# Kernel tuning notes

Measured on AMD Instinct MI355X. Metric: run time of the kernel, lower is better.

## Reference

```python
import jax, jax.numpy as jnp
import numpy as np

STATE_DIM = 2
HIDDEN = 1024
N_SKILLS = 5
N_ACTIONS = 4
BATCH = 65536


def setup_inputs() -> dict:
    key = jax.random.key(0)
    ks = jax.random.split(key, 8)
    def lin_init(k, fan_in, shape):
        bound = 1.0 / np.sqrt(fan_in)
        return jax.random.uniform(k, shape, jnp.float32, -bound, bound)
    return {
        "s": jax.random.normal(ks[0], (BATCH, STATE_DIM), jnp.float32),
        "skill_idx": jax.random.randint(ks[1], (BATCH,), 0, N_SKILLS, jnp.int32),
        "W1": lin_init(ks[2], STATE_DIM, (STATE_DIM, HIDDEN)),
        "b1": lin_init(ks[3], STATE_DIM, (HIDDEN,)),
        "W2": lin_init(ks[4], HIDDEN, (HIDDEN, HIDDEN)),
        "b2": lin_init(ks[5], HIDDEN, (HIDDEN,)),
        "W_heads": lin_init(ks[6], HIDDEN, (N_SKILLS, HIDDEN, N_ACTIONS)),
        "b_heads": lin_init(ks[7], HIDDEN, (N_SKILLS, N_ACTIONS)),
    }


def reference(s, skill_idx, W1, b1, W2, b2, W_heads, b_heads):
    # shared feature MLP: Linear -> ReLU -> Linear -> ReLU
    h = jax.nn.relu(s @ W1 + b1)            # [B, H]
    feat = jax.nn.relu(h @ W2 + b2)         # [B, H]
    # per-sample skill head: gather weights then one batched contraction
    Wg = W_heads[skill_idx]                 # [B, H, A]
    bg = b_heads[skill_idx]                 # [B, A]
    return jnp.einsum('bh,bha->ba', feat, Wg) + bg  # [B, A]
```

## Files before the change

kernel.cpp:

```cpp
#include <hip/hip_runtime.h>

typedef __bf16 bf16x8 __attribute__((ext_vector_type(8)));
typedef __bf16 bf16x4 __attribute__((ext_vector_type(4)));
typedef float  floatx4 __attribute__((ext_vector_type(4)));

#define GLOBAL_AS __attribute__((address_space(1)))
#define LOCAL_AS  __attribute__((address_space(3)))

static constexpr int HID = 1024;
static constexpr int MT  = 128;
static constexpr int BK  = 64;
static constexpr int KIT = HID / BK;

__global__ __launch_bounds__(256)
void prep_w2(const float* __restrict__ W2, __bf16* __restrict__ W2T) {
    __shared__ __bf16 tile[64][65];
    const int bx = blockIdx.x & 15;
    const int by = blockIdx.x >> 4;
    const int a  = threadIdx.x & 63;
    const int b  = threadIdx.x >> 6;
#pragma unroll
    for (int r = 0; r < 16; ++r) {
        const int k = r * 4 + b;
        tile[a][k] = (__bf16)W2[(size_t)(by * 64 + k) * HID + bx * 64 + a];
    }
    __syncthreads();
#pragma unroll
    for (int r = 0; r < 16; ++r) {
        const int n = r * 4 + b;
        const int g = a >> 3, j = a & 7;
        const int ksw = ((g ^ (n & 7)) << 3) | j;
        W2T[(size_t)(bx * 64 + n) * HID + by * 64 + ksw] = tile[n][a];
    }
}

__global__ __launch_bounds__(256)
void prep_wh(const float* __restrict__ WH, __bf16* __restrict__ WHT) {
    const int r = blockIdx.x;
    const int s = r >> 2, a = r & 3;
    for (int k = threadIdx.x; k < HID; k += 256) {
        const float v = (r < 20) ? WH[((size_t)s * HID + k) * 4 + a] : 0.f;
        const int c = k >> 7, o = (k >> 3) & 15, j = k & 7;
        const int sw = (o & 8) | ((o & 7) ^ (r & 7));
        WHT[(size_t)r * HID + c * 128 + sw * 8 + j] = (__bf16)v;
    }
}

__device__ __forceinline__ void h8(bf16x8& d, float s0, float s1,
                                   const float4& w0a, const float4& w0b,
                                   const float4& w1a, const float4& w1b,
                                   const float4& ba,  const float4& bb) {
    d[0] = (__bf16)fmaxf(fmaf(s1, w1a.x, fmaf(s0, w0a.x, ba.x)), 0.f);
    d[1] = (__bf16)fmaxf(fmaf(s1, w1a.y, fmaf(s0, w0a.y, ba.y)), 0.f);
    d[2] = (__bf16)fmaxf(fmaf(s1, w1a.z, fmaf(s0, w0a.z, ba.z)), 0.f);
    d[3] = (__bf16)fmaxf(fmaf(s1, w1a.w, fmaf(s0, w0a.w, ba.w)), 0.f);
    d[4] = (__bf16)fmaxf(fmaf(s1, w1b.x, fmaf(s0, w0b.x, bb.x)), 0.f);
    d[5] = (__bf16)fmaxf(fmaf(s1, w1b.y, fmaf(s0, w0b.y, bb.y)), 0.f);
    d[6] = (__bf16)fmaxf(fmaf(s1, w1b.z, fmaf(s0, w0b.z, bb.z)), 0.f);
    d[7] = (__bf16)fmaxf(fmaf(s1, w1b.w, fmaf(s0, w0b.w, bb.w)), 0.f);
}

__global__ __launch_bounds__(256)
void prep_h(const float* __restrict__ S, const float* __restrict__ W1,
            const float* __restrict__ B1, __bf16* __restrict__ H, int row0) {
    const int rl   = blockIdx.x * 4 + (threadIdx.x >> 6);
    const int lane = threadIdx.x & 63;
    const float s0 = S[(size_t)(row0 + rl) * 2 + 0];
    const float s1 = S[(size_t)(row0 + rl) * 2 + 1];
#pragma unroll
    for (int oo = 0; oo < 2; ++oo) {
        const int c = oo * 512 + lane * 8;
        const float4 w0a = *(const float4*)(W1 + c);
        const float4 w0b = *(const float4*)(W1 + c + 4);
        const float4 w1a = *(const float4*)(W1 + HID + c);
        const float4 w1b = *(const float4*)(W1 + HID + c + 4);
        const float4 ba  = *(const float4*)(B1 + c);
        const float4 bb  = *(const float4*)(B1 + c + 4);
        bf16x8 hv;
        h8(hv, s0, s1, w0a, w0b, w1a, w1b, ba, bb);
        const int pos = (c & ~63) | ((((c >> 3) & 7) ^ (rl & 7)) << 3);
        *(bf16x8*)(H + (size_t)rl * HID + pos) = hv;
    }
}

__global__ __launch_bounds__(256, 4)
void policy_main(const __bf16* __restrict__ H, const int* __restrict__ SK,
                 const __bf16* __restrict__ W2T, const float* __restrict__ B2,
                 const __bf16* __restrict__ WHT, const float* __restrict__ BH,
                 float* __restrict__ OUT, int row0) {
    __shared__ __align__(16) char smem[40960];
    __bf16* hA    = (__bf16*)smem;
    __bf16* Bt    = (__bf16*)(smem + 16384);
    __bf16* featL = (__bf16*)smem;
    __bf16* WHTL  = (__bf16*)(smem + 32768);

    const int tid  = threadIdx.x;
    const int lane = tid & 63;
    const int wv   = tid >> 6;
    const int wm   = wv & 1;
    const int wn   = wv >> 1;
    const int l15  = lane & 15;
    const int quad = lane >> 4;
    const int n8   = blockIdx.x & 7;
    const int i0l  = (blockIdx.x >> 3) * MT;

    floatx4 acc[4][4] = {};
    floatx4 hacc[2][2] = {};

#pragma unroll
    for (int c = 0; c < 2; ++c) {
        const int rb = c * 16 + wv * 4;
        const __bf16* gp = WHT + (size_t)(rb + (lane >> 4)) * HID
                         + n8 * 128 + (lane & 15) * 8;
        __builtin_amdgcn_global_load_lds((GLOBAL_AS void*)gp,
                                         (LOCAL_AS void*)(WHTL + rb * 128), 16, 0, 0);
    }

#pragma unroll 1
    for (int kt = 0; kt < KIT; ++kt) {
        __syncthreads();
#pragma unroll
        for (int c = 0; c < 4; ++c) {
            const int rb = c * 32 + wv * 8;
            const __bf16* gp = H + (size_t)(i0l + rb + (lane >> 3)) * HID
                             + kt * BK + (lane & 7) * 8;
            __builtin_amdgcn_global_load_lds((GLOBAL_AS void*)gp,
                                             (LOCAL_AS void*)(hA + rb * 64), 16, 0, 0);
        }
#pragma unroll
        for (int c = 0; c < 4; ++c) {
            const int rb = c * 32 + wv * 8;
            const __bf16* gp = W2T + (size_t)(n8 * 128 + rb + (lane >> 3)) * HID
                             + kt * BK + (lane & 7) * 8;
            __builtin_amdgcn_global_load_lds((GLOBAL_AS void*)gp,
                                             (LOCAL_AS void*)(Bt + rb * 64), 16, 0, 0);
        }
        __syncthreads();
#pragma unroll
        for (int ks = 0; ks < 2; ++ks) {
            bf16x8 wf[4], hf[4];
#pragma unroll
            for (int f = 0; f < 4; ++f) {
                const int row = wn * 64 + f * 16 + l15;
                wf[f] = *(const bf16x8*)(Bt + row * 64 + (((ks * 4 + quad) ^ (row & 7)) * 8));
            }
#pragma unroll
            for (int f = 0; f < 4; ++f) {
                const int smp = wm * 64 + f * 16 + l15;
                hf[f] = *(const bf16x8*)(hA + smp * 64 + (((ks * 4 + quad) ^ (smp & 7)) * 8));
            }
#pragma unroll
            for (int fn = 0; fn < 4; ++fn)
#pragma unroll
                for (int fm = 0; fm < 4; ++fm)
                    acc[fn][fm] = __builtin_amdgcn_mfma_f32_16x16x32_bf16(
                        wf[fn], hf[fm], acc[fn][fm], 0, 0, 0);
        }
    }

    __syncthreads();
#pragma unroll
    for (int fn = 0; fn < 4; ++fn) {
        const int fcb = wn * 64 + fn * 16 + quad * 4;
        const float4 b2v = *(const float4*)(B2 + n8 * 128 + fcb);
#pragma unroll
        for (int fm = 0; fm < 4; ++fm) {
            const int smp = wm * 64 + fm * 16 + l15;
            const floatx4 v = acc[fn][fm];
            bf16x4 p;
            p[0] = (__bf16)fmaxf(v[0] + b2v.x, 0.f);
            p[1] = (__bf16)fmaxf(v[1] + b2v.y, 0.f);
            p[2] = (__bf16)fmaxf(v[2] + b2v.z, 0.f);
            p[3] = (__bf16)fmaxf(v[3] + b2v.w, 0.f);
            *(bf16x4*)(featL + smp * 128 + (((fcb >> 3) ^ (smp & 15)) << 3) + (fcb & 7)) = p;
        }
    }
    __syncthreads();

#pragma unroll
    for (int f2 = 0; f2 < 2; ++f2) {
#pragma unroll
        for (int ks2 = 0; ks2 < 4; ++ks2) {
            const int row = wv * 32 + f2 * 16 + l15;
            const bf16x8 fa = *(const bf16x8*)(featL + row * 128
                                 + (((ks2 * 4 + quad) ^ (row & 15)) << 3));
#pragma unroll
            for (int t2 = 0; t2 < 2; ++t2) {
                const int r = t2 * 16 + l15;
                const int o = ks2 * 4 + quad;
                const int sw = (o & 8) | ((o & 7) ^ (r & 7));
                const bf16x8 wb = *(const bf16x8*)(WHTL + r * 128 + sw * 8);
                hacc[f2][t2] = __builtin_amdgcn_mfma_f32_16x16x32_bf16(
                    fa, wb, hacc[f2][t2], 0, 0, 0);
            }
        }
    }

#pragma unroll
    for (int f2 = 0; f2 < 2; ++f2)
#pragma unroll
        for (int j = 0; j < 4; ++j) {
            const int smp = wv * 32 + f2 * 16 + quad * 4 + j;
            const int sk  = SK[(size_t)row0 + i0l + smp];
#pragma unroll
            for (int t2 = 0; t2 < 2; ++t2) {
                const int hc = t2 * 16 + l15;
                const int d  = hc - sk * 4;
                if (d >= 0 && d < 4) {
                    float v = hacc[f2][t2][j];
                    if (n8 == 0) v += BH[hc];
                    atomicAdd(&OUT[(size_t)(row0 + i0l + smp) * 4 + d], v);
                }
            }
        }
}

extern "C" void kernel_launch(void* const* d_in, const int* in_sizes, int n_in,
                              void* d_out, int out_size, void* d_ws, size_t ws_size,
                              hipStream_t stream) {
    const float* S  = (const float*)d_in[0];
    const int*   SK = (const int*)d_in[1];
    const float* W1 = (const float*)d_in[2];
    const float* B1 = (const float*)d_in[3];
    const float* W2 = (const float*)d_in[4];
    const float* B2 = (const float*)d_in[5];
    const float* WH = (const float*)d_in[6];
    const float* BH = (const float*)d_in[7];

    char* ws = (char*)d_ws;
    __bf16* W2T = (__bf16*)ws;
    __bf16* WHT = (__bf16*)(ws + 2 * 1024 * 1024);
    __bf16* H   = (__bf16*)(ws + 2 * 1024 * 1024 + 65536);

    const size_t fixed = 2 * 1024 * 1024 + 65536;
    const size_t avail = ws_size > fixed ? ws_size - fixed : 0;
    int nc = 1;
    while (nc < 64 && (size_t)(65536 / nc) * HID * sizeof(__bf16) > avail) nc <<= 1;
    const int Mc = 65536 / nc;

    hipMemsetAsync(d_out, 0, (size_t)out_size * sizeof(float), stream);
    hipLaunchKernelGGL(prep_w2, dim3(256), dim3(256), 0, stream, W2, W2T);
    hipLaunchKernelGGL(prep_wh, dim3(32), dim3(256), 0, stream, WH, WHT);
    for (int c = 0; c < nc; ++c) {
        hipLaunchKernelGGL(prep_h, dim3(Mc / 4), dim3(256), 0, stream,
                           S, W1, B1, H, c * Mc);
        hipLaunchKernelGGL(policy_main, dim3((Mc / MT) * 8), dim3(256), 0, stream,
                           H, SK, W2T, B2, WHT, BH, (float*)d_out, c * Mc);
    }
}
```

Measured before the change: 270.9 us.

## Merge prep kernels into one launch, batch H rows per wave, remap block order

```diff
diff --git a/kernel.cpp b/kernel.cpp
--- a/kernel.cpp
+++ b/kernel.cpp
@@ -11,40 +11,6 @@
 static constexpr int MT  = 128;
 static constexpr int BK  = 64;
 static constexpr int KIT = HID / BK;
-
-__global__ __launch_bounds__(256)
-void prep_w2(const float* __restrict__ W2, __bf16* __restrict__ W2T) {
-    __shared__ __bf16 tile[64][65];
-    const int bx = blockIdx.x & 15;
-    const int by = blockIdx.x >> 4;
-    const int a  = threadIdx.x & 63;
-    const int b  = threadIdx.x >> 6;
-#pragma unroll
-    for (int r = 0; r < 16; ++r) {
-        const int k = r * 4 + b;
-        tile[a][k] = (__bf16)W2[(size_t)(by * 64 + k) * HID + bx * 64 + a];
-    }
-    __syncthreads();
-#pragma unroll
-    for (int r = 0; r < 16; ++r) {
-        const int n = r * 4 + b;
-        const int g = a >> 3, j = a & 7;
-        const int ksw = ((g ^ (n & 7)) << 3) | j;
-        W2T[(size_t)(bx * 64 + n) * HID + by * 64 + ksw] = tile[n][a];
-    }
-}
-
-__global__ __launch_bounds__(256)
-void prep_wh(const float* __restrict__ WH, __bf16* __restrict__ WHT) {
-    const int r = blockIdx.x;
-    const int s = r >> 2, a = r & 3;
-    for (int k = threadIdx.x; k < HID; k += 256) {
-        const float v = (r < 20) ? WH[((size_t)s * HID + k) * 4 + a] : 0.f;
-        const int c = k >> 7, o = (k >> 3) & 15, j = k & 7;
-        const int sw = (o & 8) | ((o & 7) ^ (r & 7));
-        WHT[(size_t)r * HID + c * 128 + sw * 8 + j] = (__bf16)v;
-    }
-}
 
 __device__ __forceinline__ void h8(bf16x8& d, float s0, float s1,
                                    const float4& w0a, const float4& w0b,
@@ -61,25 +27,68 @@
 }
 
 __global__ __launch_bounds__(256)
-void prep_h(const float* __restrict__ S, const float* __restrict__ W1,
-            const float* __restrict__ B1, __bf16* __restrict__ H, int row0) {
-    const int rl   = blockIdx.x * 4 + (threadIdx.x >> 6);
-    const int lane = threadIdx.x & 63;
-    const float s0 = S[(size_t)(row0 + rl) * 2 + 0];
-    const float s1 = S[(size_t)(row0 + rl) * 2 + 1];
-#pragma unroll
-    for (int oo = 0; oo < 2; ++oo) {
-        const int c = oo * 512 + lane * 8;
-        const float4 w0a = *(const float4*)(W1 + c);
-        const float4 w0b = *(const float4*)(W1 + c + 4);
-        const float4 w1a = *(const float4*)(W1 + HID + c);
-        const float4 w1b = *(const float4*)(W1 + HID + c + 4);
-        const float4 ba  = *(const float4*)(B1 + c);
-        const float4 bb  = *(const float4*)(B1 + c + 4);
-        bf16x8 hv;
-        h8(hv, s0, s1, w0a, w0b, w1a, w1b, ba, bb);
-        const int pos = (c & ~63) | ((((c >> 3) & 7) ^ (rl & 7)) << 3);
-        *(bf16x8*)(H + (size_t)rl * HID + pos) = hv;
+void prep_all(const float* __restrict__ S,  const float* __restrict__ W1,
+              const float* __restrict__ B1, const float* __restrict__ W2,
+              const float* __restrict__ WH,
+              __bf16* __restrict__ H, __bf16* __restrict__ W2T,
+              __bf16* __restrict__ WHT, int row0, int nh) {
+    if (blockIdx.x < (unsigned)nh) {
+        const int wid  = blockIdx.x * 4 + (threadIdx.x >> 6);
+        const int lane = threadIdx.x & 63;
+        const int rb   = wid * 8;
+        float2 sv[8];
+#pragma unroll
+        for (int r = 0; r < 8; ++r)
+            sv[r] = *(const float2*)(S + (size_t)(row0 + rb + r) * 2);
+#pragma unroll
+        for (int oo = 0; oo < 2; ++oo) {
+            const int c = oo * 512 + lane * 8;
+            const float4 w0a = *(const float4*)(W1 + c);
+            const float4 w0b = *(const float4*)(W1 + c + 4);
+            const float4 w1a = *(const float4*)(W1 + HID + c);
+            const float4 w1b = *(const float4*)(W1 + HID + c + 4);
+            const float4 ba  = *(const float4*)(B1 + c);
+            const float4 bb  = *(const float4*)(B1 + c + 4);
+#pragma unroll
+            for (int r = 0; r < 8; ++r) {
+                const int rl = rb + r;
+                bf16x8 hv;
+                h8(hv, sv[r].x, sv[r].y, w0a, w0b, w1a, w1b, ba, bb);
+                const int pos = (c & ~63) | ((((c >> 3) & 7) ^ (rl & 7)) << 3);
+                *(bf16x8*)(H + (size_t)rl * HID + pos) = hv;
+            }
+        }
+        return;
+    }
+    const int b = blockIdx.x - nh;
+    if (b < 256) {
+        __shared__ __bf16 tile[64][65];
+        const int bx = b & 15;
+        const int by = b >> 4;
+        const int a  = threadIdx.x & 63;
+        const int bb = threadIdx.x >> 6;
+#pragma unroll
+        for (int r = 0; r < 16; ++r) {
+            const int k = r * 4 + bb;
+            tile[a][k] = (__bf16)W2[(size_t)(by * 64 + k) * HID + bx * 64 + a];
+        }
+        __syncthreads();
+#pragma unroll
+        for (int r = 0; r < 16; ++r) {
+            const int n = r * 4 + bb;
+            const int g = a >> 3, j = a & 7;
+            const int ksw = ((g ^ (n & 7)) << 3) | j;
+            W2T[(size_t)(bx * 64 + n) * HID + by * 64 + ksw] = tile[n][a];
+        }
+    } else {
+        const int r = b - 256;
+        const int s = r >> 2, a = r & 3;
+        for (int k = threadIdx.x; k < HID; k += 256) {
+            const float v = (r < 20) ? WH[((size_t)s * HID + k) * 4 + a] : 0.f;
+            const int c = k >> 7, o = (k >> 3) & 15, j = k & 7;
+            const int sw = (o & 8) | ((o & 7) ^ (r & 7));
+            WHT[(size_t)r * HID + c * 128 + sw * 8 + j] = (__bf16)v;
+        }
     }
 }
 
@@ -87,7 +96,7 @@
 void policy_main(const __bf16* __restrict__ H, const int* __restrict__ SK,
                  const __bf16* __restrict__ W2T, const float* __restrict__ B2,
                  const __bf16* __restrict__ WHT, const float* __restrict__ BH,
-                 float* __restrict__ OUT, int row0) {
+                 float* __restrict__ OUT, int row0, int mg_bits) {
     __shared__ __align__(16) char smem[40960];
     __bf16* hA    = (__bf16*)smem;
     __bf16* Bt    = (__bf16*)(smem + 16384);
@@ -101,8 +110,8 @@
     const int wn   = wv >> 1;
     const int l15  = lane & 15;
     const int quad = lane >> 4;
-    const int n8   = blockIdx.x & 7;
-    const int i0l  = (blockIdx.x >> 3) * MT;
+    const int n8   = blockIdx.x >> mg_bits;
+    const int i0l  = (blockIdx.x & ((1 << mg_bits) - 1)) * MT;
 
     floatx4 acc[4][4] = {};
     floatx4 hacc[2][2] = {};
@@ -237,14 +246,16 @@
     int nc = 1;
     while (nc < 64 && (size_t)(65536 / nc) * HID * sizeof(__bf16) > avail) nc <<= 1;
     const int Mc = 65536 / nc;
+    int mg_bits = 0;
+    while ((1 << mg_bits) < Mc / MT) ++mg_bits;
 
     hipMemsetAsync(d_out, 0, (size_t)out_size * sizeof(float), stream);
-    hipLaunchKernelGGL(prep_w2, dim3(256), dim3(256), 0, stream, W2, W2T);
-    hipLaunchKernelGGL(prep_wh, dim3(32), dim3(256), 0, stream, WH, WHT);
     for (int c = 0; c < nc; ++c) {
-        hipLaunchKernelGGL(prep_h, dim3(Mc / 4), dim3(256), 0, stream,
-                           S, W1, B1, H, c * Mc);
+        const int nh = Mc / 32;
+        const int extra = (c == 0) ? 288 : 0;
+        hipLaunchKernelGGL(prep_all, dim3(nh + extra), dim3(256), 0, stream,
+                           S, W1, B1, W2, WH, H, W2T, WHT, c * Mc, nh);
         hipLaunchKernelGGL(policy_main, dim3((Mc / MT) * 8), dim3(256), 0, stream,
-                           H, SK, W2T, B2, WHT, BH, (float*)d_out, c * Mc);
-    }
-}
+                           H, SK, W2T, B2, WHT, BH, (float*)d_out, c * Mc, mg_bits);
+    }
+}
```

New measurement: 252.5 us. 1.07x faster.
